# Kernel optimization log

Hardware: AMD Instinct MI355X
Metric: run time of the kernel (lower is better)

The kernel has to match this reference:

```python
import jax, jax.numpy as jnp
import numpy as np
from jax import lax

HEADS = 8
WIN_SIZES = (2, 4, 8)


def _linear(x, w, b):
    return x @ w + b


def _window_attention(x2d, ws, w4, b4):
    # x2d: (B,H,W,C); w4: (4,C,C) = [q,k,v,out]; b4: (4,C)
    B, H, W, C = x2d.shape
    p1, p2 = H // ws, W // ws
    xw = x2d.reshape(B, p1, ws, p2, ws, C).transpose(0, 1, 3, 2, 4, 5)
    xw = xw.reshape(B, p1, p2, ws * ws, C)
    hs = C // HEADS
    q = _linear(xw, w4[0], b4[0]).reshape(B, p1, p2, ws * ws, HEADS, hs)
    k = _linear(xw, w4[1], b4[1]).reshape(B, p1, p2, ws * ws, HEADS, hs)
    v = _linear(xw, w4[2], b4[2]).reshape(B, p1, p2, ws * ws, HEADS, hs)
    scores = jnp.einsum('bpqwhd,bpqvhd->bpqhwv', q, k) / jnp.sqrt(jnp.asarray(hs, x2d.dtype))
    probs = jax.nn.softmax(scores, axis=-1)
    ctx = jnp.einsum('bpqhwv,bpqvhd->bpqwhd', probs, v).reshape(B, p1, p2, ws * ws, C)
    return _linear(ctx, w4[3], b4[3])


def _unwindow(out, ws):
    B, p1, p2, win, C = out.shape
    s = out.reshape(B, p1, p2, ws, ws, C).transpose(0, 1, 3, 2, 4, 5)
    return s.reshape(B, p1 * ws, p2 * ws, C)


def _up_bilinear_ac(x, oh, ow):
    # x: (B,C,h,w); bilinear with align_corners=True (UpsamplingBilinear2d)
    B, C, h, w = x.shape
    def grid(o, i):
        pos = jnp.arange(o, dtype=x.dtype) * ((i - 1) / (o - 1))
        i0 = jnp.floor(pos).astype(jnp.int32)
        i1 = jnp.minimum(i0 + 1, i - 1)
        return i0, i1, pos - i0.astype(x.dtype)
    r0, r1, tr = grid(oh, h)
    c0, c1, tc = grid(ow, w)
    xr = x[:, :, r0, :] * (1 - tr)[None, None, :, None] + x[:, :, r1, :] * tr[None, None, :, None]
    return xr[:, :, :, c0] * (1 - tc) + xr[:, :, :, c1] * tc


def _forward(x, attn_w, attn_b, edge_w, mlp_w1, mlp_b1, mlp_w2, mlp_b2,
             dl_w, dl_b, ax_w, ax_b, g_shift, g_bias, sq_w, sq_b):
    B, N, C = x.shape
    H = W = int(np.sqrt(N))
    x2d = x.reshape(B, H, W, C)

    # multi-scale window attention branches
    scale_outputs = [_unwindow(_window_attention(x2d, ws, attn_w[i], attn_b[i]), ws)
                     for i, ws in enumerate(WIN_SIZES)]

    # adaptive window selector
    xc = x2d.transpose(0, 3, 1, 2)  # (B,C,H,W)
    edge = jnp.abs(lax.conv_general_dilated(xc, edge_w, (1, 1), 'SAME'))
    avg = lax.reduce_window(edge, 0.0, lax.add, (1, 1, 3, 3), (1, 1, 1, 1), 'SAME') / 9.0
    e = avg.transpose(0, 2, 3, 1)  # (B,H,W,1)
    wts = jax.nn.softmax(jax.nn.relu(e @ mlp_w1 + mlp_b1) @ mlp_w2 + mlp_b2, axis=-1)

    blended = sum(wts[..., i:i + 1] * scale_outputs[i] for i in range(len(WIN_SIZES)))
    h_map = blended.transpose(0, 3, 1, 2)  # (B,C,H,W)

    # ws=4 window attention -> DlightConv token pooling
    x_win = _window_attention(x2d, 4, attn_w[1], attn_b[1])  # (B,p,p,16,C)
    probs = jax.nn.softmax(jnp.mean(x_win, axis=-2) @ dl_w + dl_b, axis=-1)
    x_dl = jnp.sum(x_win * probs[..., None], axis=-2)  # (B,p,p,C)

    # axial attention (no head split, no scaling in the axial branch)
    q = _linear(x_dl, ax_w[0], ax_b[0])
    k = _linear(x_dl, ax_w[1], ax_b[1])
    v = _linear(x_dl, ax_w[2], ax_b[2])
    scores_x = jnp.einsum('bhwc,bhvc->bhwv', q, k)  # (B,r,c,k)
    scores_y = jnp.einsum('bhwc,bvwc->bwhv', q, k)  # (B,c,r,k)

    # GaussianTrans: vectorized per-pixel gaussian positional bias
    p = x_dl.shape[1]
    idx = jnp.arange(p, dtype=x.dtype)
    dist2 = (idx[None, :] - idx[:, None]) ** 2          # [pos, k]
    gb = -(g_shift[0] * dist2 + g_bias[0])              # (p,p)
    ax = jax.nn.softmax(scores_x + gb[None, None, :, :], axis=-1)       # bias indexed by c
    ay = jax.nn.softmax(jnp.swapaxes(scores_y, 1, 2) + gb[None, :, None, :], axis=-1)  # bias by r
    x_g = jnp.einsum('brck,brkd->brcd', ax, v) + jnp.einsum('brck,bkcd->brcd', ay, v)

    x_g = _up_bilinear_ac(x_g.transpose(0, 3, 1, 2), H, W)  # (B,C,H,W)

    cat = jnp.concatenate([x_g, h_map], axis=1)  # (B,2C,H,W)
    out = jnp.einsum('oc,bchw->bohw', sq_w, cat) + sq_b[None, :, None, None]
    return out.transpose(0, 2, 3, 1).reshape(B, N, C)


def setup_inputs() -> dict:
    key = jax.random.key(0)
    ks = jax.random.split(key, 16)
    B, N, C = 16, 4096, 256
    s = 0.02
    return {
        'x': jax.random.normal(ks[0], (B, N, C), jnp.float32),
        'attn_w': jax.random.normal(ks[1], (3, 4, C, C), jnp.float32) * s,
        'attn_b': jax.random.normal(ks[2], (3, 4, C), jnp.float32) * s,
        'edge_w': jax.random.normal(ks[3], (1, C, 3, 3), jnp.float32) * s,
        'mlp_w1': jax.random.normal(ks[4], (1, 16), jnp.float32) * s,
        'mlp_b1': jax.random.normal(ks[5], (16,), jnp.float32) * s,
        'mlp_w2': jax.random.normal(ks[6], (16, 3), jnp.float32) * s,
        'mlp_b2': jax.random.normal(ks[7], (3,), jnp.float32) * s,
        'dl_w': jax.random.normal(ks[8], (C, 16), jnp.float32) * s,
        'dl_b': jax.random.normal(ks[9], (16,), jnp.float32) * s,
        'ax_w': jax.random.normal(ks[10], (3, C, C), jnp.float32) * s,
        'ax_b': jax.random.normal(ks[11], (3, C), jnp.float32) * s,
        'g_shift': jnp.abs(jax.random.normal(ks[12], (1,), jnp.float32)),
        'g_bias': -jnp.abs(jax.random.normal(ks[13], (1,), jnp.float32)),
        'sq_w': jax.random.normal(ks[14], (C, 2 * C), jnp.float32) * s,
        'sq_b': jax.random.normal(ks[15], (C,), jnp.float32) * s,
    }


def reference(x, attn_w, attn_b, edge_w, mlp_w1, mlp_b1, mlp_w2, mlp_b2,
              dl_w, dl_b, ax_w, ax_b, g_shift, g_bias, sq_w, sq_b):
    return _forward(x, attn_w, attn_b, edge_w, mlp_w1, mlp_b1, mlp_w2, mlp_b2,
                    dl_w, dl_b, ax_w, ax_b, g_shift, g_bias, sq_w, sq_b)
```

## Files before the change

### kernel.cpp

```cpp
#include <hip/hip_runtime.h>
#include <math.h>


#define CHUNK_B 4
#define CHUNK_TOK (CHUNK_B * 4096)
#define KS 32

typedef __attribute__((ext_vector_type(8))) short short8;
typedef __attribute__((ext_vector_type(8))) unsigned short ushort8;
typedef __attribute__((ext_vector_type(4))) float f32x4;

__device__ __forceinline__ ushort f2bf(float f) {
    union { float f; unsigned u; } v; v.f = f;
    unsigned r = v.u + 0x7fff + ((v.u >> 16) & 1);
    return (ushort)(r >> 16);
}
__device__ __forceinline__ float bf2f(ushort h) {
    union { unsigned u; float f; } v; v.u = ((unsigned)h) << 16; return v.f;
}
__device__ __forceinline__ void split2(float v, ushort& h, ushort& l) {
    h = f2bf(v);
    l = f2bf(v - bf2f(h));
}

__device__ __forceinline__ void gld16(const ushort* g, ushort* l) {
    __builtin_amdgcn_global_load_lds(
        (const __attribute__((address_space(1))) unsigned int*)g,
        (__attribute__((address_space(3))) unsigned int*)l,
        16, 0, 0);
}

__global__ __launch_bounds__(256) void split_w_kmajor(
    const float* __restrict__ W, ushort* __restrict__ Th, ushort* __restrict__ Tl, int nmats)
{
    const int idx = blockIdx.x * 256 + threadIdx.x;
    if (idx >= nmats * 65536) return;
    const int mat = idx >> 16, r = idx & 65535;
    const int n = r >> 8, k = r & 255;
    const float v = W[(size_t)mat * 65536 + k * 256 + n];
    ushort h, l; split2(v, h, l);
    Th[idx] = h; Tl[idx] = l;
}
__global__ __launch_bounds__(256) void split_w_nmajor(
    const float* __restrict__ W, ushort* __restrict__ Th, ushort* __restrict__ Tl, int total)
{
    const int idx = blockIdx.x * 256 + threadIdx.x;
    if (idx >= total) return;
    ushort h, l; split2(W[idx], h, l);
    Th[idx] = h; Tl[idx] = l;
}

#define GEMM_DECLS                                                            \
    __shared__ ushort Ah[128 * KS], Al[128 * KS], Bh[128 * KS], Bl[128 * KS]; \
    const int tid = threadIdx.x;                                              \
    const int wave = tid >> 6, lane = tid & 63;                               \
    const int quad = lane >> 4, l16 = lane & 15;                              \
    const int wr = (wave >> 1) * 64, wc = (wave & 1) * 64;                    \
    f32x4 acc[4][4];                                                          \
    _Pragma("unroll") for (int i = 0; i < 4; i++)                             \
        _Pragma("unroll") for (int j = 0; j < 4; j++)                         \
            acc[i][j] = (f32x4){0.f, 0.f, 0.f, 0.f};

#define STAGE_GLD(dstbuf, srcp, strideE, rowbase, k0e)                        \
    _Pragma("unroll") for (int jj = 0; jj < 2; jj++) {                        \
        const int rr = (wave << 5) + (jj << 4) + (lane >> 2);                 \
        const int kqs = (lane & 3) ^ ((lane >> 3) & 3);                       \
        gld16((srcp) + (size_t)((rowbase) + rr) * (strideE) + (k0e) + (kqs << 3), \
              (dstbuf) + (wave << 10) + (jj << 9));                           \
    }

#define STAGE_F32(AhD, AlD, Aptr, kk)                                         \
    _Pragma("unroll") for (int cc = 0; cc < 2; cc++) {                        \
        const int ch = tid + cc * 256;                                        \
        const int r = ch >> 2, kq = ch & 3;                                   \
        const int wsl = (kq ^ ((r >> 1) & 3)) * 8;                            \
        const float* p = (Aptr) + (size_t)(m0 + r) * 256 + (kk) + kq * 8;     \
        const float4 v0 = *(const float4*)p;                                  \
        const float4 v1 = *(const float4*)(p + 4);                            \
        ushort8 h, l; ushort hh, ll;                                          \
        split2(v0.x, hh, ll); h[0] = hh; l[0] = ll;                           \
        split2(v0.y, hh, ll); h[1] = hh; l[1] = ll;                           \
        split2(v0.z, hh, ll); h[2] = hh; l[2] = ll;                           \
        split2(v0.w, hh, ll); h[3] = hh; l[3] = ll;                           \
        split2(v1.x, hh, ll); h[4] = hh; l[4] = ll;                           \
        split2(v1.y, hh, ll); h[5] = hh; l[5] = ll;                           \
        split2(v1.z, hh, ll); h[6] = hh; l[6] = ll;                           \
        split2(v1.w, hh, ll); h[7] = hh; l[7] = ll;                           \
        *(ushort8*)&(AhD)[r * KS + wsl] = h;                                  \
        *(ushort8*)&(AlD)[r * KS + wsl] = l;                                  \
    }

#define GEMM_COMPUTE                                                          \
    {                                                                         \
        const int aswz = (l16 & 6) << 2;                  \
        short8 afh[4], afl[4], bfh[4], bfl[4];                                \
        _Pragma("unroll") for (int i = 0; i < 4; i++) {                       \
            const int ro = (wr + i * 16 + l16) * KS + ((quad * 8) ^ aswz);    \
            afh[i] = *(const short8*)&Ah[ro];                                 \
            afl[i] = *(const short8*)&Al[ro];                                 \
        }                                                                     \
        _Pragma("unroll") for (int j = 0; j < 4; j++) {                       \
            const int no = (wc + j * 16 + l16) * KS + ((quad * 8) ^ aswz);    \
            bfh[j] = *(const short8*)&Bh[no];                                 \
            bfl[j] = *(const short8*)&Bl[no];                                 \
        }                                                                     \
        _Pragma("unroll") for (int i = 0; i < 4; i++)                         \
            _Pragma("unroll") for (int j = 0; j < 4; j++) {                   \
                acc[i][j] = __builtin_amdgcn_mfma_f32_16x16x32_bf16(          \
                    afh[i], bfh[j], acc[i][j], 0, 0, 0);                      \
                acc[i][j] = __builtin_amdgcn_mfma_f32_16x16x32_bf16(          \
                    afl[i], bfh[j], acc[i][j], 0, 0, 0);                      \
                acc[i][j] = __builtin_amdgcn_mfma_f32_16x16x32_bf16(          \
                    afh[i], bfl[j], acc[i][j], 0, 0, 0);                      \
            }                                                                 \
    }

__global__ __launch_bounds__(256, 2) void gemm3_mfma(
    const ushort* __restrict__ AgH, const ushort* __restrict__ AgL,
    const ushort* __restrict__ Wth, const ushort* __restrict__ Wtl,
    const float* __restrict__ b0, const float* __restrict__ b1, const float* __restrict__ b2,
    float* __restrict__ O0, float* __restrict__ O1, float* __restrict__ O2)
{
    const int m0 = blockIdx.x * 128;
    const int mat = blockIdx.y >> 1;
    const int col0 = (blockIdx.y & 1) * 128;
    const ushort* wth = Wth + (size_t)mat * 65536 + (size_t)col0 * 256;
    const ushort* wtl = Wtl + (size_t)mat * 65536 + (size_t)col0 * 256;
    GEMM_DECLS
    for (int k0 = 0; k0 < 256; k0 += 32) {
        STAGE_GLD(Ah, AgH, 256, m0, k0)
        STAGE_GLD(Al, AgL, 256, m0, k0)
        STAGE_GLD(Bh, wth, 256, 0, k0)
        STAGE_GLD(Bl, wtl, 256, 0, k0)
        __syncthreads();
        GEMM_COMPUTE
        __syncthreads();
    }
    const float* bias = (mat == 0) ? b0 : (mat == 1) ? b1 : b2;
    float* O = (mat == 0) ? O0 : (mat == 1) ? O1 : O2;
#pragma unroll
    for (int j = 0; j < 4; j++) {
        const int col = col0 + wc + j * 16 + l16;
        const float bj = bias[col];
#pragma unroll
        for (int i = 0; i < 4; i++) {
            const int rbase = m0 + wr + i * 16 + quad * 4;
#pragma unroll
            for (int r = 0; r < 4; r++)
                O[(size_t)(rbase + r) * 256 + col] = acc[i][j][r] + bj;
        }
    }
}

__global__ __launch_bounds__(256, 2) void gemmp_mfma(
    const ushort* __restrict__ AgH, const ushort* __restrict__ AgL,
    const ushort* __restrict__ Wth, const ushort* __restrict__ Wtl,
    const float* __restrict__ bias,
    float* __restrict__ Sout, int store_s,
    float* __restrict__ Blnd, const float* __restrict__ wts, int scale_idx, int blend_init,
    int row_off)
{
    const int m0 = blockIdx.x * 128;
    const int col0 = blockIdx.y * 128;
    const ushort* wth = Wth + (size_t)col0 * 256;
    const ushort* wtl = Wtl + (size_t)col0 * 256;
    GEMM_DECLS
    for (int k0 = 0; k0 < 256; k0 += 32) {
        STAGE_GLD(Ah, AgH, 256, m0, k0)
        STAGE_GLD(Al, AgL, 256, m0, k0)
        STAGE_GLD(Bh, wth, 256, 0, k0)
        STAGE_GLD(Bl, wtl, 256, 0, k0)
        __syncthreads();
        GEMM_COMPUTE
        __syncthreads();
    }
#pragma unroll
    for (int i = 0; i < 4; i++) {
        const int rbase = m0 + wr + i * 16 + quad * 4;
#pragma unroll
        for (int r = 0; r < 4; r++) {
            const size_t grow = (size_t)row_off + rbase + r;
            const float wt = wts[grow * 3 + scale_idx];
#pragma unroll
            for (int j = 0; j < 4; j++) {
                const int col = col0 + wc + j * 16 + l16;
                const float v = acc[i][j][r] + bias[col];
                if (store_s) Sout[grow * 256 + col] = v;
                float* bp = Blnd + grow * 256 + col;
                if (blend_init) *bp = wt * v;
                else            *bp = *bp + wt * v;
            }
        }
    }
}

__global__ __launch_bounds__(256, 2) void gemmf_mfma(
    const ushort* __restrict__ UPH, const ushort* __restrict__ UPL,
    const float* __restrict__ BLD,
    const ushort* __restrict__ Wth, const ushort* __restrict__ Wtl,
    const float* __restrict__ SQB, float* __restrict__ OUT)
{
    const int m0 = blockIdx.x * 128;
    const int col0 = blockIdx.y * 128;
    const ushort* wth = Wth + (size_t)col0 * 512;
    const ushort* wtl = Wtl + (size_t)col0 * 512;
    GEMM_DECLS
    for (int k0 = 0; k0 < 512; k0 += 32) {
        if (k0 < 256) {
            STAGE_GLD(Ah, UPH, 256, m0, k0)
            STAGE_GLD(Al, UPL, 256, m0, k0)
        } else {
            STAGE_F32(Ah, Al, BLD, (k0 & 255))
        }
        STAGE_GLD(Bh, wth, 512, 0, k0)
        STAGE_GLD(Bl, wtl, 512, 0, k0)
        __syncthreads();
        GEMM_COMPUTE
        __syncthreads();
    }
#pragma unroll
    for (int j = 0; j < 4; j++) {
        const int col = col0 + wc + j * 16 + l16;
        const float bj = SQB[col];
#pragma unroll
        for (int i = 0; i < 4; i++) {
            const int rbase = m0 + wr + i * 16 + quad * 4;
#pragma unroll
            for (int r = 0; r < 4; r++)
                OUT[(size_t)(rbase + r) * 256 + col] = acc[i][j][r] + bj;
        }
    }
}

template <int WS, int NH>
__global__ __launch_bounds__(256) void win_attn(
    const float* __restrict__ Q, const float* __restrict__ K,
    const float* __restrict__ V, ushort* __restrict__ CTXh, ushort* __restrict__ CTXl)
{
    constexpr int WIN = WS * WS;
    constexpr int NW = 64 / WS;
    constexpr int CW = NH * 32;
    __shared__ float qs[WIN][CW + 4], ks[WIN][CW + 4], vs[WIN][CW + 4];
    __shared__ float sc[NH][WIN][WIN + 1];
    const int tid = threadIdx.x;
    const int wid = blockIdx.x;
    const int b = wid / (NW * NW);
    const int rem = wid % (NW * NW);
    const int p = rem / NW, q = rem % NW;
    const int h0 = blockIdx.y * NH;

    for (int idx = tid; idx < WIN * CW; idx += 256) {
        const int i = idx / CW;
        const int cc = idx % CW;
        const int ti = i / WS, tj = i % WS;
        const size_t g = ((size_t)(b * 4096 + (p * WS + ti) * 64 + (q * WS + tj))) * 256 + h0 * 32 + cc;
        qs[i][cc] = Q[g]; ks[i][cc] = K[g]; vs[i][cc] = V[g];
    }
    __syncthreads();
    const float scale = 0.17677669529663687f;
    for (int idx = tid; idx < NH * WIN * WIN; idx += 256) {
        const int hl = idx / (WIN * WIN);
        const int r = idx % (WIN * WIN);
        const int i = r / WIN, j = r % WIN;
        const int co = hl * 32;
        float s = 0.f;
#pragma unroll
        for (int d = 0; d < 32; d++) s += qs[i][co + d] * ks[j][co + d];
        sc[hl][i][j] = s * scale;
    }
    __syncthreads();
    if (tid < NH * WIN) {
        const int hl = tid / WIN, i = tid % WIN;
        float mx = -3.4e38f;
        for (int j = 0; j < WIN; j++) mx = fmaxf(mx, sc[hl][i][j]);
        float sum = 0.f;
        for (int j = 0; j < WIN; j++) {
            float e = __expf(sc[hl][i][j] - mx);
            sc[hl][i][j] = e; sum += e;
        }
        const float inv = 1.f / sum;
        for (int j = 0; j < WIN; j++) sc[hl][i][j] *= inv;
    }
    __syncthreads();
    for (int idx = tid; idx < WIN * CW; idx += 256) {
        const int i = idx / CW;
        const int cc = idx % CW;
        const int hl = cc >> 5;
        float s = 0.f;
        for (int j = 0; j < WIN; j++) s += sc[hl][i][j] * vs[j][cc];
        const int ti = i / WS, tj = i % WS;
        const size_t g = ((size_t)(b * 4096 + (p * WS + ti) * 64 + (q * WS + tj))) * 256 + h0 * 32 + cc;
        ushort hh, ll; split2(s, hh, ll);
        CTXh[g] = hh; CTXl[g] = ll;
    }
}

__global__ __launch_bounds__(256) void edge_gemm9(
    const float* __restrict__ x, const float* __restrict__ ew, float* __restrict__ ytmp,
    ushort* __restrict__ Xh, ushort* __restrict__ Xl)
{
    __shared__ float wsm[2304];
    const int tid = threadIdx.x;
    for (int i = tid; i < 2304; i += 256) wsm[i] = ew[i];
    __syncthreads();
    const int wave = tid >> 6, lane = tid & 63;
    const int p = blockIdx.x * 4 + wave;
    const float4 xv = *(const float4*)(x + (size_t)p * 256 + lane * 4);
    {
        ushort4 h4, l4;
        split2(xv.x, h4.x, l4.x); split2(xv.y, h4.y, l4.y);
        split2(xv.z, h4.z, l4.z); split2(xv.w, h4.w, l4.w);
        *(ushort4*)(Xh + (size_t)p * 256 + lane * 4) = h4;
        *(ushort4*)(Xl + (size_t)p * 256 + lane * 4) = l4;
    }
    float acc[9];
#pragma unroll
    for (int t = 0; t < 9; t++) acc[t] = 0.f;
    const float xs[4] = {xv.x, xv.y, xv.z, xv.w};
#pragma unroll
    for (int i = 0; i < 4; i++) {
        const int c = lane * 4 + i;
#pragma unroll
        for (int t = 0; t < 9; t++)
            acc[t] = fmaf(xs[i], wsm[c * 9 + t], acc[t]);
    }
#pragma unroll
    for (int t = 0; t < 9; t++) {
#pragma unroll
        for (int off = 1; off < 64; off <<= 1)
            acc[t] += __shfl_xor(acc[t], off);
    }
    if (lane < 9) {
        float v = acc[0];
        switch (lane) {
            case 1: v = acc[1]; break; case 2: v = acc[2]; break;
            case 3: v = acc[3]; break; case 4: v = acc[4]; break;
            case 5: v = acc[5]; break; case 6: v = acc[6]; break;
            case 7: v = acc[7]; break; case 8: v = acc[8]; break;
            default: break;
        }
        ytmp[(size_t)p * 9 + lane] = v;
    }
}

__global__ __launch_bounds__(256) void edge_combine(
    const float* __restrict__ ytmp, float* __restrict__ edge)
{
    const int idx = blockIdx.x * 256 + threadIdx.x;
    const int b = idx >> 12, rem = idx & 4095, h = rem >> 6, w = rem & 63;
    float s = 0.f;
#pragma unroll
    for (int kh = 0; kh < 3; kh++) {
        const int hh = h + kh - 1;
        if ((unsigned)hh > 63u) continue;
#pragma unroll
        for (int kw = 0; kw < 3; kw++) {
            const int ww = w + kw - 1;
            if ((unsigned)ww > 63u) continue;
            s += ytmp[((size_t)b * 4096 + hh * 64 + ww) * 9 + kh * 3 + kw];
        }
    }
    edge[idx] = fabsf(s);
}

__global__ __launch_bounds__(256) void avg_mlp(
    const float* __restrict__ edge, const float* __restrict__ w1, const float* __restrict__ b1,
    const float* __restrict__ w2, const float* __restrict__ b2, float* __restrict__ wts)
{
    const int idx = blockIdx.x * 256 + threadIdx.x;
    const int b = idx >> 12, rem = idx & 4095, h = rem >> 6, w = rem & 63;
    float s = 0.f;
#pragma unroll
    for (int kh = -1; kh <= 1; kh++) {
        const int hh = h + kh;
        if ((unsigned)hh > 63u) continue;
#pragma unroll
        for (int kw = -1; kw <= 1; kw++) {
            const int ww = w + kw;
            if ((unsigned)ww > 63u) continue;
            s += edge[(size_t)b * 4096 + hh * 64 + ww];
        }
    }
    const float e = s / 9.f;
    float l0 = b2[0], l1 = b2[1], l2 = b2[2];
#pragma unroll
    for (int j = 0; j < 16; j++) {
        float hd = fmaxf(e * w1[j] + b1[j], 0.f);
        l0 += hd * w2[j * 3 + 0];
        l1 += hd * w2[j * 3 + 1];
        l2 += hd * w2[j * 3 + 2];
    }
    const float mx = fmaxf(l0, fmaxf(l1, l2));
    const float e0 = __expf(l0 - mx), e1 = __expf(l1 - mx), e2 = __expf(l2 - mx);
    const float inv = 1.f / (e0 + e1 + e2);
    wts[(size_t)idx * 3 + 0] = e0 * inv;
    wts[(size_t)idx * 3 + 1] = e1 * inv;
    wts[(size_t)idx * 3 + 2] = e2 * inv;
}

__global__ __launch_bounds__(256) void dlight(
    const float* __restrict__ S1, const float* __restrict__ dlw,
    const float* __restrict__ dlb, ushort* __restrict__ XDLH, ushort* __restrict__ XDLL)
{
    __shared__ float xw[16][257];
    __shared__ float m[256];
    __shared__ float pr[16];
    __shared__ float pr2[16];
    const int wid = blockIdx.x;
    const int b = wid >> 8, rem = wid & 255, p = rem >> 4, q = rem & 15;
    const int tid = threadIdx.x;
#pragma unroll
    for (int t = 0; t < 16; t++) {
        const int ti = t >> 2, tj = t & 3;
        xw[t][tid] = S1[((size_t)b * 4096 + (p * 4 + ti) * 64 + (q * 4 + tj)) * 256 + tid];
    }
    float mm = 0.f;
#pragma unroll
    for (int t = 0; t < 16; t++) mm += xw[t][tid];
    m[tid] = mm * (1.f / 16.f);
    __syncthreads();
    if (tid < 16) {
        float lg = dlb[tid];
        for (int c = 0; c < 256; c++) lg += m[c] * dlw[c * 16 + tid];
        pr[tid] = lg;
    }
    __syncthreads();
    if (tid < 16) {
        float mx = -3.4e38f;
        for (int j = 0; j < 16; j++) mx = fmaxf(mx, pr[j]);
        float sum = 0.f;
        for (int j = 0; j < 16; j++) sum += __expf(pr[j] - mx);
        pr2[tid] = __expf(pr[tid] - mx) / sum;
    }
    __syncthreads();
    float o = 0.f;
#pragma unroll
    for (int t = 0; t < 16; t++) o += xw[t][tid] * pr2[t];
    ushort hh, ll; split2(o, hh, ll);
    XDLH[(size_t)wid * 256 + tid] = hh;
    XDLL[(size_t)wid * 256 + tid] = ll;
}

__global__ __launch_bounds__(256) void axial_row(
    const float* __restrict__ Q, const float* __restrict__ K, const float* __restrict__ V,
    const float* __restrict__ gsp, const float* __restrict__ gbp, float* __restrict__ XG)
{
    __shared__ float qs[16][257], ks[16][257], vs[16][257];
    __shared__ float sc[16][17];
    const int bid = blockIdx.x;
    const int b = bid >> 4, r = bid & 15;
    const int tid = threadIdx.x;
    const float gs = gsp[0], gb = gbp[0];
#pragma unroll
    for (int w = 0; w < 16; w++) {
        const size_t base = ((size_t)b * 256 + r * 16 + w) * 256 + tid;
        qs[w][tid] = Q[base]; ks[w][tid] = K[base]; vs[w][tid] = V[base];
    }
    __syncthreads();
    {
        const int w = tid >> 4, vv = tid & 15;
        float s = 0.f;
        for (int c = 0; c < 256; c++) s += qs[w][c] * ks[vv][c];
        const float d = (float)(w - vv);
        sc[w][vv] = s - (gs * d * d + gb);
    }
    __syncthreads();
    if (tid < 16) {
        float mx = -3.4e38f;
        for (int j = 0; j < 16; j++) mx = fmaxf(mx, sc[tid][j]);
        float sum = 0.f;
        for (int j = 0; j < 16; j++) {
            float e = __expf(sc[tid][j] - mx);
            sc[tid][j] = e; sum += e;
        }
        const float inv = 1.f / sum;
        for (int j = 0; j < 16; j++) sc[tid][j] *= inv;
    }
    __syncthreads();
#pragma unroll
    for (int w2 = 0; w2 < 16; w2++) {
        float o = 0.f;
#pragma unroll
        for (int k2 = 0; k2 < 16; k2++) o += sc[w2][k2] * vs[k2][tid];
        XG[((size_t)b * 256 + r * 16 + w2) * 256 + tid] = o;
    }
}

__global__ __launch_bounds__(256) void axial_col(
    const float* __restrict__ Q, const float* __restrict__ K, const float* __restrict__ V,
    const float* __restrict__ gsp, const float* __restrict__ gbp, float* __restrict__ XG)
{
    __shared__ float qs[16][257], ks[16][257], vs[16][257];
    __shared__ float sc[16][17];
    const int bid = blockIdx.x;
    const int b = bid >> 4, col = bid & 15;
    const int tid = threadIdx.x;
    const float gs = gsp[0], gb = gbp[0];
#pragma unroll
    for (int h = 0; h < 16; h++) {
        const size_t base = ((size_t)b * 256 + h * 16 + col) * 256 + tid;
        qs[h][tid] = Q[base]; ks[h][tid] = K[base]; vs[h][tid] = V[base];
    }
    __syncthreads();
    {
        const int r = tid >> 4, vv = tid & 15;
        float s = 0.f;
        for (int c = 0; c < 256; c++) s += qs[r][c] * ks[vv][c];
        const float d = (float)(r - vv);
        sc[r][vv] = s - (gs * d * d + gb);
    }
    __syncthreads();
    if (tid < 16) {
        float mx = -3.4e38f;
        for (int j = 0; j < 16; j++) mx = fmaxf(mx, sc[tid][j]);
        float sum = 0.f;
        for (int j = 0; j < 16; j++) {
            float e = __expf(sc[tid][j] - mx);
            sc[tid][j] = e; sum += e;
        }
        const float inv = 1.f / sum;
        for (int j = 0; j < 16; j++) sc[tid][j] *= inv;
    }
    __syncthreads();
#pragma unroll
    for (int r2 = 0; r2 < 16; r2++) {
        float o = 0.f;
#pragma unroll
        for (int k2 = 0; k2 < 16; k2++) o += sc[r2][k2] * vs[k2][tid];
        XG[((size_t)b * 256 + r2 * 16 + col) * 256 + tid] += o;
    }
}

__global__ __launch_bounds__(256) void upsample(
    const float* __restrict__ XG, ushort* __restrict__ UPH, ushort* __restrict__ UPL)
{
    const unsigned idx = blockIdx.x * 256u + threadIdx.x;
    const int c = idx & 255;
    const unsigned t2 = idx >> 8;
    const int w = t2 & 63;
    const unsigned t3 = t2 >> 6;
    const int h = t3 & 63;
    const int b = t3 >> 6;
    const float rr = 15.f / 63.f;
    const float ph = h * rr, pw = w * rr;
    int h0 = (int)floorf(ph); float th = ph - (float)h0; int h1 = min(h0 + 1, 15);
    int w0 = (int)floorf(pw); float tw = pw - (float)w0; int w1 = min(w0 + 1, 15);
    const size_t bb = (size_t)b * 256;
    const float v00 = XG[((bb + h0 * 16 + w0)) * 256 + c];
    const float v10 = XG[((bb + h1 * 16 + w0)) * 256 + c];
    const float v01 = XG[((bb + h0 * 16 + w1)) * 256 + c];
    const float v11 = XG[((bb + h1 * 16 + w1)) * 256 + c];
    const float c0 = v00 * (1.f - th) + v10 * th;
    const float c1 = v01 * (1.f - th) + v11 * th;
    const float val = c0 * (1.f - tw) + c1 * tw;
    ushort hh, ll; split2(val, hh, ll);
    UPH[idx] = hh; UPL[idx] = ll;
}

extern "C" void kernel_launch(void* const* d_in, const int* in_sizes, int n_in,
                              void* d_out, int out_size, void* d_ws, size_t ws_size,
                              hipStream_t stream)
{
    const float* x      = (const float*)d_in[0];
    const float* attn_w = (const float*)d_in[1];
    const float* attn_b = (const float*)d_in[2];
    const float* edge_w = (const float*)d_in[3];
    const float* mlp_w1 = (const float*)d_in[4];
    const float* mlp_b1 = (const float*)d_in[5];
    const float* mlp_w2 = (const float*)d_in[6];
    const float* mlp_b2 = (const float*)d_in[7];
    const float* dl_w   = (const float*)d_in[8];
    const float* dl_b   = (const float*)d_in[9];
    const float* ax_w   = (const float*)d_in[10];
    const float* ax_b   = (const float*)d_in[11];
    const float* g_shift= (const float*)d_in[12];
    const float* g_bias = (const float*)d_in[13];
    const float* sq_w   = (const float*)d_in[14];
    const float* sq_b   = (const float*)d_in[15];
    float* out = (float*)d_out;

    float* ws = (float*)d_ws;
    const size_t MT = 65536;
    float* blend = ws;
    float* s1    = blend + MT * 256;
    float* scr   = s1 + MT * 256;
    float* chQ   = scr;
    float* chK   = chQ + (size_t)CHUNK_TOK * 256;
    float* chV   = chK + (size_t)CHUNK_TOK * 256;
    ushort* ctxh = (ushort*)(chV + (size_t)CHUNK_TOK * 256);
    ushort* ctxl = ctxh + (size_t)CHUNK_TOK * 256;
    ushort* uph  = (ushort*)scr;
    ushort* upl  = uph + MT * 256;
    float* ytmp  = scr;
    float* edge  = scr + MT * 256;
    float* wts   = edge + 65536;
    float* xdl   = wts + 196608;
    ushort* xdlh = (ushort*)xdl;
    ushort* xdll = xdlh + 1048576;
    float* axq   = xdl + 1048576;
    float* axk   = axq + 1048576;
    float* axv   = axk + 1048576;
    float* xg    = axv + 1048576;
    ushort* Wth = (ushort*)(xg + 1048576);
    ushort* Wtl = Wth + 1114112;
    ushort* xh = (ushort*)out;
    ushort* xl = xh + MT * 256;

    split_w_kmajor<<<(12 * 65536 + 255) / 256, 256, 0, stream>>>(attn_w, Wth, Wtl, 12);
    split_w_kmajor<<<(3 * 65536 + 255) / 256, 256, 0, stream>>>(
        ax_w, Wth + (size_t)12 * 65536, Wtl + (size_t)12 * 65536, 3);
    split_w_nmajor<<<(131072 + 255) / 256, 256, 0, stream>>>(
        sq_w, Wth + (size_t)15 * 65536, Wtl + (size_t)15 * 65536, 131072);

    edge_gemm9<<<16384, 256, 0, stream>>>(x, edge_w, ytmp, xh, xl);
    edge_combine<<<256, 256, 0, stream>>>(ytmp, edge);
    avg_mlp<<<256, 256, 0, stream>>>(edge, mlp_w1, mlp_b1, mlp_w2, mlp_b2, wts);

    for (int i = 0; i < 3; i++) {
        const ushort* Wh = Wth + (size_t)i * 4 * 65536;
        const ushort* Wl = Wtl + (size_t)i * 4 * 65536;
        const float* c0 = attn_b + (size_t)(i * 4 + 0) * 256;
        const float* c1 = attn_b + (size_t)(i * 4 + 1) * 256;
        const float* c2 = attn_b + (size_t)(i * 4 + 2) * 256;
        const float* c3 = attn_b + (size_t)(i * 4 + 3) * 256;
        for (int ch = 0; ch < 16 / CHUNK_B; ch++) {
            const size_t toff = (size_t)ch * CHUNK_TOK;
            gemm3_mfma<<<dim3(CHUNK_TOK / 128, 6), 256, 0, stream>>>(
                xh + toff * 256, xl + toff * 256, Wh, Wl, c0, c1, c2, chQ, chK, chV);
            if (i == 0)
                win_attn<2, 8><<<dim3(CHUNK_B * 32 * 32, 1), 256, 0, stream>>>(chQ, chK, chV, ctxh, ctxl);
            if (i == 1)
                win_attn<4, 4><<<dim3(CHUNK_B * 16 * 16, 2), 256, 0, stream>>>(chQ, chK, chV, ctxh, ctxl);
            if (i == 2)
                win_attn<8, 1><<<dim3(CHUNK_B * 8 * 8, 8), 256, 0, stream>>>(chQ, chK, chV, ctxh, ctxl);
            gemmp_mfma<<<dim3(CHUNK_TOK / 128, 2), 256, 0, stream>>>(
                ctxh, ctxl, Wh + (size_t)3 * 65536, Wl + (size_t)3 * 65536, c3,
                s1, (i == 1) ? 1 : 0, blend, wts, i, (i == 0) ? 1 : 0, (int)toff);
        }
    }

    dlight<<<4096, 256, 0, stream>>>(s1, dl_w, dl_b, xdlh, xdll);

    gemm3_mfma<<<dim3(4096 / 128, 6), 256, 0, stream>>>(
        xdlh, xdll, Wth + (size_t)12 * 65536, Wtl + (size_t)12 * 65536,
        ax_b, ax_b + 256, ax_b + 512, axq, axk, axv);
    axial_row<<<256, 256, 0, stream>>>(axq, axk, axv, g_shift, g_bias, xg);
    axial_col<<<256, 256, 0, stream>>>(axq, axk, axv, g_shift, g_bias, xg);

    upsample<<<65536, 256, 0, stream>>>(xg, uph, upl);

    gemmf_mfma<<<dim3(512, 2), 256, 0, stream>>>(
        uph, upl, blend, Wth + (size_t)15 * 65536, Wtl + (size_t)15 * 65536, sq_b, out);
}
```

Before: 1.300 ms.

## Register-prefetch GEMM tiles and swap chunk/scale loop order

Replaces direct global-to-LDS async loads in the three MFMA GEMM kernels with register-staged prefetch: the next K-slice is loaded into registers while the current slice is computed, then written to LDS. The fp32 path in the final GEMM is likewise split into a load step and a split-and-store step. The host loop is reordered so each token chunk runs all three window scales back-to-back, which may improve cache reuse of the chunk's input. Register pressure rises and could lower occupancy, and the ordering of the blend accumulation across scales changes.

```diff
diff --git a/kernel.cpp b/kernel.cpp
--- a/kernel.cpp
+++ b/kernel.cpp
@@ -21,13 +21,6 @@
 __device__ __forceinline__ void split2(float v, ushort& h, ushort& l) {
     h = f2bf(v);
     l = f2bf(v - bf2f(h));
-}
-
-__device__ __forceinline__ void gld16(const ushort* g, ushort* l) {
-    __builtin_amdgcn_global_load_lds(
-        (const __attribute__((address_space(1))) unsigned int*)g,
-        (__attribute__((address_space(3))) unsigned int*)l,
-        16, 0, 0);
 }
 
 __global__ __launch_bounds__(256) void split_w_kmajor(
@@ -61,22 +54,33 @@
         _Pragma("unroll") for (int j = 0; j < 4; j++)                         \
             acc[i][j] = (f32x4){0.f, 0.f, 0.f, 0.f};
 
-#define STAGE_GLD(dstbuf, srcp, strideE, rowbase, k0e)                        \
-    _Pragma("unroll") for (int jj = 0; jj < 2; jj++) {                        \
-        const int rr = (wave << 5) + (jj << 4) + (lane >> 2);                 \
-        const int kqs = (lane & 3) ^ ((lane >> 3) & 3);                       \
-        gld16((srcp) + (size_t)((rowbase) + rr) * (strideE) + (k0e) + (kqs << 3), \
-              (dstbuf) + (wave << 10) + (jj << 9));                           \
-    }
-
-#define STAGE_F32(AhD, AlD, Aptr, kk)                                         \
+#define LD_US(reg, src, strideE, rowbase, k0e)                                \
     _Pragma("unroll") for (int cc = 0; cc < 2; cc++) {                        \
-        const int ch = tid + cc * 256;                                        \
-        const int r = ch >> 2, kq = ch & 3;                                   \
-        const int wsl = (kq ^ ((r >> 1) & 3)) * 8;                            \
-        const float* p = (Aptr) + (size_t)(m0 + r) * 256 + (kk) + kq * 8;     \
-        const float4 v0 = *(const float4*)p;                                  \
-        const float4 v1 = *(const float4*)(p + 4);                            \
+        const int ch_ = tid + cc * 256;                                       \
+        const int r_ = ch_ >> 2;                                              \
+        const int kq_ = (ch_ & 3) ^ ((r_ >> 1) & 3);                          \
+        reg[cc] = *(const ushort8*)((src) +                                   \
+            (size_t)((rowbase) + r_) * (strideE) + (k0e) + (kq_ << 3));       \
+    }
+#define WR_US(dst, reg)                                                       \
+    _Pragma("unroll") for (int cc = 0; cc < 2; cc++) {                        \
+        *(ushort8*)&(dst)[(tid + cc * 256) * 8] = reg[cc];                    \
+    }
+
+#define LD_F32(Aptr, kk)                                                      \
+    {                                                                         \
+        const int r0_ = tid >> 2, kc_ = (tid & 3) * 8;                        \
+        const float* p0 = (Aptr) + (size_t)(m0 + r0_) * 256 + (kk) + kc_;     \
+        const float* p1 = p0 + (size_t)64 * 256;                              \
+        va[0] = *(const float4*)p0; va[1] = *(const float4*)(p0 + 4);         \
+        va[2] = *(const float4*)p1; va[3] = *(const float4*)(p1 + 4);         \
+    }
+#define WR_F32(AhD, AlD)                                                      \
+    _Pragma("unroll") for (int cc = 0; cc < 2; cc++) {                        \
+        const int r_ = (tid >> 2) + cc * 64;                                  \
+        const int kq_ = tid & 3;                                              \
+        const int wsl_ = (kq_ ^ ((r_ >> 1) & 3)) << 3;                        \
+        const float4 v0 = va[cc * 2], v1 = va[cc * 2 + 1];                    \
         ushort8 h, l; ushort hh, ll;                                          \
         split2(v0.x, hh, ll); h[0] = hh; l[0] = ll;                           \
         split2(v0.y, hh, ll); h[1] = hh; l[1] = ll;                           \
@@ -86,8 +90,8 @@
         split2(v1.y, hh, ll); h[5] = hh; l[5] = ll;                           \
         split2(v1.z, hh, ll); h[6] = hh; l[6] = ll;                           \
         split2(v1.w, hh, ll); h[7] = hh; l[7] = ll;                           \
-        *(ushort8*)&(AhD)[r * KS + wsl] = h;                                  \
-        *(ushort8*)&(AlD)[r * KS + wsl] = l;                                  \
+        *(ushort8*)&(AhD)[r_ * KS + wsl_] = h;                                \
+        *(ushort8*)&(AlD)[r_ * KS + wsl_] = l;                                \
     }
 
 #define GEMM_COMPUTE                                                          \
@@ -127,14 +131,25 @@
     const ushort* wth = Wth + (size_t)mat * 65536 + (size_t)col0 * 256;
     const ushort* wtl = Wtl + (size_t)mat * 65536 + (size_t)col0 * 256;
     GEMM_DECLS
-    for (int k0 = 0; k0 < 256; k0 += 32) {
-        STAGE_GLD(Ah, AgH, 256, m0, k0)
-        STAGE_GLD(Al, AgL, 256, m0, k0)
-        STAGE_GLD(Bh, wth, 256, 0, k0)
-        STAGE_GLD(Bl, wtl, 256, 0, k0)
+    ushort8 raH[2], raL[2], rbH[2], rbL[2];
+    LD_US(raH, AgH, 256, m0, 0)
+    LD_US(raL, AgL, 256, m0, 0)
+    LD_US(rbH, wth, 256, 0, 0)
+    LD_US(rbL, wtl, 256, 0, 0)
+#pragma unroll
+    for (int t = 0; t < 8; ++t) {
         __syncthreads();
+        WR_US(Ah, raH) WR_US(Al, raL)
+        WR_US(Bh, rbH) WR_US(Bl, rbL)
+        __syncthreads();
+        if (t < 7) {
+            const int k1 = (t + 1) * 32;
+            LD_US(raH, AgH, 256, m0, k1)
+            LD_US(raL, AgL, 256, m0, k1)
+            LD_US(rbH, wth, 256, 0, k1)
+            LD_US(rbL, wtl, 256, 0, k1)
+        }
         GEMM_COMPUTE
-        __syncthreads();
     }
     const float* bias = (mat == 0) ? b0 : (mat == 1) ? b1 : b2;
     float* O = (mat == 0) ? O0 : (mat == 1) ? O1 : O2;
@@ -165,14 +180,25 @@
     const ushort* wth = Wth + (size_t)col0 * 256;
     const ushort* wtl = Wtl + (size_t)col0 * 256;
     GEMM_DECLS
-    for (int k0 = 0; k0 < 256; k0 += 32) {
-        STAGE_GLD(Ah, AgH, 256, m0, k0)
-        STAGE_GLD(Al, AgL, 256, m0, k0)
-        STAGE_GLD(Bh, wth, 256, 0, k0)
-        STAGE_GLD(Bl, wtl, 256, 0, k0)
+    ushort8 raH[2], raL[2], rbH[2], rbL[2];
+    LD_US(raH, AgH, 256, m0, 0)
+    LD_US(raL, AgL, 256, m0, 0)
+    LD_US(rbH, wth, 256, 0, 0)
+    LD_US(rbL, wtl, 256, 0, 0)
+#pragma unroll
+    for (int t = 0; t < 8; ++t) {
         __syncthreads();
+        WR_US(Ah, raH) WR_US(Al, raL)
+        WR_US(Bh, rbH) WR_US(Bl, rbL)
+        __syncthreads();
+        if (t < 7) {
+            const int k1 = (t + 1) * 32;
+            LD_US(raH, AgH, 256, m0, k1)
+            LD_US(raL, AgL, 256, m0, k1)
+            LD_US(rbH, wth, 256, 0, k1)
+            LD_US(rbL, wtl, 256, 0, k1)
+        }
         GEMM_COMPUTE
-        __syncthreads();
     }
 #pragma unroll
     for (int i = 0; i < 4; i++) {
@@ -205,18 +231,31 @@
     const ushort* wth = Wth + (size_t)col0 * 512;
     const ushort* wtl = Wtl + (size_t)col0 * 512;
     GEMM_DECLS
-    for (int k0 = 0; k0 < 512; k0 += 32) {
-        if (k0 < 256) {
-            STAGE_GLD(Ah, UPH, 256, m0, k0)
-            STAGE_GLD(Al, UPL, 256, m0, k0)
-        } else {
-            STAGE_F32(Ah, Al, BLD, (k0 & 255))
-        }
-        STAGE_GLD(Bh, wth, 512, 0, k0)
-        STAGE_GLD(Bl, wtl, 512, 0, k0)
+    ushort8 raH[2], raL[2], rbH[2], rbL[2];
+    float4 va[4];
+    LD_US(raH, UPH, 256, m0, 0)
+    LD_US(raL, UPL, 256, m0, 0)
+    LD_US(rbH, wth, 512, 0, 0)
+    LD_US(rbL, wtl, 512, 0, 0)
+#pragma unroll
+    for (int t = 0; t < 16; ++t) {
         __syncthreads();
+        if (t < 8) { WR_US(Ah, raH) WR_US(Al, raL) }
+        else       { WR_F32(Ah, Al) }
+        WR_US(Bh, rbH) WR_US(Bl, rbL)
+        __syncthreads();
+        if (t < 15) {
+            const int k1 = (t + 1) * 32;
+            LD_US(rbH, wth, 512, 0, k1)
+            LD_US(rbL, wtl, 512, 0, k1)
+            if (k1 < 256) {
+                LD_US(raH, UPH, 256, m0, k1)
+                LD_US(raL, UPL, 256, m0, k1)
+            } else {
+                LD_F32(BLD, (k1 & 255))
+            }
+        }
         GEMM_COMPUTE
-        __syncthreads();
     }
 #pragma unroll
     for (int j = 0; j < 4; j++) {
@@ -616,15 +655,15 @@
     edge_combine<<<256, 256, 0, stream>>>(ytmp, edge);
     avg_mlp<<<256, 256, 0, stream>>>(edge, mlp_w1, mlp_b1, mlp_w2, mlp_b2, wts);
 
-    for (int i = 0; i < 3; i++) {
-        const ushort* Wh = Wth + (size_t)i * 4 * 65536;
-        const ushort* Wl = Wtl + (size_t)i * 4 * 65536;
-        const float* c0 = attn_b + (size_t)(i * 4 + 0) * 256;
-        const float* c1 = attn_b + (size_t)(i * 4 + 1) * 256;
-        const float* c2 = attn_b + (size_t)(i * 4 + 2) * 256;
-        const float* c3 = attn_b + (size_t)(i * 4 + 3) * 256;
-        for (int ch = 0; ch < 16 / CHUNK_B; ch++) {
-            const size_t toff = (size_t)ch * CHUNK_TOK;
+    for (int ch = 0; ch < 16 / CHUNK_B; ch++) {
+        const size_t toff = (size_t)ch * CHUNK_TOK;
+        for (int i = 0; i < 3; i++) {
+            const ushort* Wh = Wth + (size_t)i * 4 * 65536;
+            const ushort* Wl = Wtl + (size_t)i * 4 * 65536;
+            const float* c0 = attn_b + (size_t)(i * 4 + 0) * 256;
+            const float* c1 = attn_b + (size_t)(i * 4 + 1) * 256;
+            const float* c2 = attn_b + (size_t)(i * 4 + 2) * 256;
+            const float* c3 = attn_b + (size_t)(i * 4 + 3) * 256;
             gemm3_mfma<<<dim3(CHUNK_TOK / 128, 6), 256, 0, stream>>>(
                 xh + toff * 256, xl + toff * 256, Wh, Wl, c0, c1, c2, chQ, chK, chV);
             if (i == 0)
```

New measurement: 1.282 ms. Within noise of the previous version (-1.4%).
